# Kernel optimization log

Measured on AMD Instinct MI355X. Metric: run time of the kernel, lower is better.

## Reference

```python
import jax, jax.numpy as jnp
import numpy as np

N = 100000   # points in scan
K = 20       # KNN neighbors
D = 96       # backbone feature dim
H = 1024     # random-projection dim
C = 7        # num classes


def setup_inputs() -> dict:
    key = jax.random.key(0)
    ks = jax.random.split(key, 6)
    feat_source = jax.random.normal(ks[0], (N, D), jnp.float32)
    proto = jax.random.normal(ks[1], (C, D), jnp.float32)
    w_rand = jax.random.normal(ks[2], (D, H), jnp.float32)
    Q = jnp.zeros((H, C), jnp.float32)
    G = jnp.zeros((H, H), jnp.float32)
    coords = jax.random.normal(ks[3], (N, 3), jnp.float32) * 30.0
    normals_z = jax.random.uniform(ks[4], (N,), jnp.float32)
    near_indices = jax.random.randint(ks[5], (N, K), 0, N).astype(jnp.int64)
    return dict(feat_source=feat_source, proto=proto, w_rand=w_rand, Q=Q, G=G,
                coords=coords, normals_z=normals_z, near_indices=near_indices)


def _prior_filter(preds, coords, normals_z):
    plane_pred = (preds == 2) | (preds == 3) | (preds == 4)
    manmade_pred = preds == 5
    other = (preds == 0) | (preds == 1) | (preds == 6)
    ground = plane_pred & (normals_z > 0.9) & (coords[:, 2] < -10.0)
    g_index = ground | other | manmade_pred
    m_index = (manmade_pred & (normals_z < 0.1)) | other | plane_pred
    return g_index, m_index


def reference(feat_source, proto, w_rand, Q, G, coords, normals_z, near_indices):
    RIDGE = 100.0  # stand-in for optimise_ridge_parameter (source not provided)
    # prototype logits: feat @ normalize(proto, dim=1).T   [N, C]
    proto_n = proto / jnp.maximum(jnp.linalg.norm(proto, axis=1, keepdims=True), 1e-12)
    pred_proto = feat_source @ proto_n.T
    preds = jnp.argmax(pred_proto, axis=1)                       # [N]
    # KNN consistency filtering (irregular gather)
    neigh = preds[near_indices]                                  # [N, K]
    consistency = jnp.mean((neigh == preds[:, None]).astype(jnp.float32), axis=1)
    cmask = consistency > 0.8
    g_index, m_index = _prior_filter(preds, coords, normals_z)
    mask = cmask & g_index & m_index                             # [N]
    # random-projection features
    feat_h = jax.nn.relu(feat_source @ w_rand)                   # [N, H]
    yhat = jax.nn.one_hot(preds, C, dtype=feat_h.dtype)          # [N, C]
    mw = mask.astype(feat_h.dtype)[:, None]
    fh_m = feat_h * mw                                           # masked rows (mask^2 == mask)
    Qn = Q + jnp.einsum('nh,nc->hc', fh_m, yhat)
    Gn = G + fh_m.T @ fh_m
    # ridge solve: wo = solve(G + r*I, Q); module does feat_h @ wo
    wo = jnp.linalg.solve(Gn + RIDGE * jnp.eye(H, dtype=Gn.dtype), Qn)  # [H, C]
    pred_domain = feat_h @ wo                                    # [N, C]
    return pred_domain
```

## Files before the change

### kernel.cpp

```cpp
#include <hip/hip_runtime.h>

#define D_DIM 96
#define K_NN  20
#define H_DIM 1024
#define C_CLS 7


__global__ void k_preds(const float* __restrict__ feat,
                        const float* __restrict__ proto,
                        const long long* __restrict__ idx_ll,
                        int* __restrict__ preds, int* __restrict__ flags, int N) {
  __shared__ float pn[C_CLS * D_DIM];
  __shared__ float inv[C_CLS];
  __shared__ int any_big;
  if (threadIdx.x == 0) any_big = 0;
  if (threadIdx.x < C_CLS) {
    float ss = 0.f;
    for (int d = 0; d < D_DIM; d++) {
      float v = proto[threadIdx.x * D_DIM + d];
      ss += v * v;
    }
    inv[threadIdx.x] = 1.0f / fmaxf(sqrtf(ss), 1e-12f);
  }
  __syncthreads();
  for (int j = threadIdx.x; j < C_CLS * D_DIM; j += blockDim.x)
    pn[j] = proto[j] * inv[j / D_DIM];
  if (blockIdx.x == 0) {
    for (int j = threadIdx.x; j < 1024; j += blockDim.x) {
      long long v = idx_ll[j];
      if (v < 0 || v >= N) any_big = 1;
    }
  }
  __syncthreads();
  if (blockIdx.x == 0 && threadIdx.x == 0) {
    flags[0] = 0;
    flags[1] = any_big ? 0 : 1;
  }
  int i = blockIdx.x * blockDim.x + threadIdx.x;
  if (i >= N) return;
  const float4* fp = (const float4*)(feat + (size_t)i * D_DIM);
  float s[C_CLS];
#pragma unroll
  for (int c = 0; c < C_CLS; c++) s[c] = 0.f;
#pragma unroll
  for (int q = 0; q < D_DIM / 4; q++) {
    float4 v = fp[q];
    int d = q * 4;
#pragma unroll
    for (int c = 0; c < C_CLS; c++) {
      s[c] += v.x * pn[c * D_DIM + d]     + v.y * pn[c * D_DIM + d + 1]
            + v.z * pn[c * D_DIM + d + 2] + v.w * pn[c * D_DIM + d + 3];
    }
  }
  float best = s[0]; int bi = 0;
#pragma unroll
  for (int c = 1; c < C_CLS; c++) { if (s[c] > best) { best = s[c]; bi = c; } }
  preds[i] = bi;
}

__global__ void k_mask(const int* __restrict__ preds, const void* __restrict__ nearv,
                       const float* __restrict__ coords, const float* __restrict__ normz,
                       int* __restrict__ flags, int* __restrict__ list, int N) {
  int i = blockIdx.x * blockDim.x + threadIdx.x;
  if (i >= N) return;
  int p = preds[i];
  int cnt = 0;
  if (flags[1]) {
    const long long* nn = (const long long*)nearv + (long long)i * K_NN;
#pragma unroll
    for (int k = 0; k < K_NN; k++) cnt += (preds[(int)nn[k]] == p) ? 1 : 0;
  } else {
    const int* nn = (const int*)nearv + (size_t)i * K_NN;
#pragma unroll
    for (int k = 0; k < K_NN; k++) cnt += (preds[nn[k]] == p) ? 1 : 0;
  }
  bool cmask = (cnt >= 17);
  bool plane = (p == 2) || (p == 3) || (p == 4);
  bool man   = (p == 5);
  bool other = (p == 0) || (p == 1) || (p == 6);
  float nz = normz[i];
  bool ground = plane && (nz > 0.9f) && (coords[(size_t)i * 3 + 2] < -10.0f);
  bool g = ground || other || man;
  bool m = (man && (nz < 0.1f)) || other || plane;
  if (cmask && g && m) {
    int pos = atomicAdd(&flags[0], 1);
    list[pos] = i;
  }
}

__global__ void k_qn_copy(const float* __restrict__ feat, const float* __restrict__ w,
                          const float* __restrict__ Q, const int* __restrict__ preds,
                          const int* __restrict__ flags, const int* __restrict__ list,
                          float* __restrict__ Qn,
                          const float* __restrict__ G, float* __restrict__ Gn) {
  if (blockIdx.x < 1024) {
    size_t t = (size_t)blockIdx.x * 256 + threadIdx.x;
    ((float4*)Gn)[t] = ((const float4*)G)[t];
    return;
  }
  int h = (blockIdx.x - 1024) * 256 + threadIdx.x;
  float q[C_CLS];
#pragma unroll
  for (int c = 0; c < C_CLS; c++) q[c] = Q[h * C_CLS + c];
  int M = flags[0];
  for (int m = 0; m < M; m++) {
    int i = list[m];
    float s = 0.f;
    for (int d = 0; d < D_DIM; d++) s += feat[(size_t)i * D_DIM + d] * w[(size_t)d * H_DIM + h];
    s = fmaxf(s, 0.f);
    q[preds[i]] += s;
  }
#pragma unroll
  for (int c = 0; c < C_CLS; c++) Qn[h * C_CLS + c] = q[c];
}

__global__ void k_gram_acc(const float* __restrict__ feat, const float* __restrict__ w,
                           const int* __restrict__ flags, const int* __restrict__ list,
                           float* __restrict__ Gn) {
  int M = flags[0];
  if (M == 0) return;
  int bx = blockIdx.x & 15, by = blockIdx.x >> 4;
  int tr0 = by * 64, tc0 = bx * 64;
  __shared__ float fr[64], fc[64], fsh[D_DIM];
  float acc[4][4];
#pragma unroll
  for (int u = 0; u < 4; u++)
#pragma unroll
    for (int v = 0; v < 4; v++) acc[u][v] = 0.f;
  int t = threadIdx.x;
  int tu = t >> 4, tv = t & 15;
  for (int m = 0; m < M; m++) {
    int i = list[m];
    if (t < D_DIM) fsh[t] = feat[(size_t)i * D_DIM + t];
    __syncthreads();
    if (t < 64) {
      float s = 0.f;
      for (int d = 0; d < D_DIM; d++) s += fsh[d] * w[(size_t)d * H_DIM + tr0 + t];
      fr[t] = fmaxf(s, 0.f);
    } else if (t < 128) {
      int c = t - 64;
      float s = 0.f;
      for (int d = 0; d < D_DIM; d++) s += fsh[d] * w[(size_t)d * H_DIM + tc0 + c];
      fc[c] = fmaxf(s, 0.f);
    }
    __syncthreads();
#pragma unroll
    for (int u = 0; u < 4; u++)
#pragma unroll
      for (int v = 0; v < 4; v++) acc[u][v] += fr[tu * 4 + u] * fc[tv * 4 + v];
    __syncthreads();
  }
#pragma unroll
  for (int u = 0; u < 4; u++)
#pragma unroll
    for (int v = 0; v < 4; v++) {
      int r = tr0 + tu * 4 + u, c = tc0 + tv * 4 + v;
      Gn[(size_t)r * H_DIM + c] += acc[u][v];
    }
}

__device__ inline void block_reduce7(const float* val, volatile float* out,
                                     float* red) {
  int lane = threadIdx.x & 63, wave = threadIdx.x >> 6;
#pragma unroll
  for (int c = 0; c < C_CLS; c++) {
    float v = val[c];
#pragma unroll
    for (int o = 32; o > 0; o >>= 1) v += __shfl_down(v, o, 64);
    if (lane == 0) red[wave * C_CLS + c] = v;
  }
  __syncthreads();
  if (threadIdx.x == 0) {
#pragma unroll
    for (int c = 0; c < C_CLS; c++) {
      float s = 0.f;
      for (int wv = 0; wv < 16; wv++) s += red[wv * C_CLS + c];
      out[c] = s;
    }
  }
  __syncthreads();
}

__global__ void __launch_bounds__(1024) k_solve(const float* __restrict__ Gn,
                                                const float* __restrict__ Qn,
                                                float* __restrict__ wo,
                                                float* __restrict__ wo_flag) {
  const int h = threadIdx.x;
  __shared__ float psh[H_DIM * C_CLS];
  __shared__ float red[16 * C_CLS];
  __shared__ float rs[C_CLS], bn2[C_CLS], pap[C_CLS], rsn[C_CLS];

  float x[C_CLS], r[C_CLS], p[C_CLS], t7[C_CLS];
#pragma unroll
  for (int c = 0; c < C_CLS; c++) {
    float b = Qn[h * C_CLS + c];
    x[c] = 0.f; r[c] = b; p[c] = b;
    t7[c] = b * b;
  }
  block_reduce7(t7, rs, red);
  if (h == 0) {
#pragma unroll
    for (int c = 0; c < C_CLS; c++) bn2[c] = rs[c];
  }
  __syncthreads();

  for (int it = 0; it < H_DIM; it++) {
    bool done = true;
#pragma unroll
    for (int c = 0; c < C_CLS; c++)
      done = done && (rs[c] <= bn2[c] * 1e-16f + 1e-30f);
    if (done) break;

#pragma unroll
    for (int c = 0; c < C_CLS; c++) psh[h * C_CLS + c] = p[c];
    __syncthreads();

    float ap[C_CLS];
#pragma unroll
    for (int c = 0; c < C_CLS; c++) ap[c] = 100.0f * p[c];
    const float* grow = Gn + (size_t)h * H_DIM;
    for (int k = 0; k < H_DIM; k++) {
      float g = grow[k];
#pragma unroll
      for (int c = 0; c < C_CLS; c++) ap[c] += g * psh[k * C_CLS + c];
    }
#pragma unroll
    for (int c = 0; c < C_CLS; c++) t7[c] = p[c] * ap[c];
    block_reduce7(t7, pap, red);

    float a[C_CLS], rsold[C_CLS];
#pragma unroll
    for (int c = 0; c < C_CLS; c++) {
      rsold[c] = rs[c];
      bool act = rs[c] > bn2[c] * 1e-16f + 1e-30f;
      a[c] = act ? rsold[c] / fmaxf(pap[c], 1e-37f) : 0.f;
    }
#pragma unroll
    for (int c = 0; c < C_CLS; c++) {
      x[c] += a[c] * p[c];
      r[c] -= a[c] * ap[c];
      t7[c] = r[c] * r[c];
    }
    block_reduce7(t7, rsn, red);
#pragma unroll
    for (int c = 0; c < C_CLS; c++) {
      float bb = rsn[c] / fmaxf(rsold[c], 1e-37f);
      p[c] = r[c] + bb * p[c];
    }
    if (h == 0) {
#pragma unroll
      for (int c = 0; c < C_CLS; c++) rs[c] = rsn[c];
    }
    __syncthreads();
  }

#pragma unroll
  for (int c = 0; c < C_CLS; c++) wo[h * C_CLS + c] = x[c];
  float s = 0.f;
#pragma unroll
  for (int c = 0; c < C_CLS; c++) s += fabsf(x[c]);
  t7[0] = s;
#pragma unroll
  for (int c = 1; c < C_CLS; c++) t7[c] = 0.f;
  block_reduce7(t7, rsn, red);
  if (h == 0) *wo_flag = rsn[0];
}

__global__ void k_out(const float* __restrict__ feat, const float* __restrict__ w,
                      const float* __restrict__ wo, const float* __restrict__ wo_flag,
                      float* __restrict__ out, int N) {
  if (*wo_flag == 0.0f) {
    long long tid = (long long)blockIdx.x * blockDim.x + threadIdx.x;
    long long total = (long long)N * C_CLS;
    if (tid < total) out[tid] = 0.0f;
    return;
  }
  int i = blockIdx.x * blockDim.x + threadIdx.x;
  if (i >= N) return;
  float f[D_DIM];
  const float4* fp = (const float4*)(feat + (size_t)i * D_DIM);
#pragma unroll
  for (int q = 0; q < D_DIM / 4; q++) {
    float4 v = fp[q];
    f[4 * q] = v.x; f[4 * q + 1] = v.y; f[4 * q + 2] = v.z; f[4 * q + 3] = v.w;
  }
  float acc[C_CLS];
#pragma unroll
  for (int c = 0; c < C_CLS; c++) acc[c] = 0.f;
  for (int hh = 0; hh < H_DIM; hh++) {
    float s = 0.f;
#pragma unroll 8
    for (int d = 0; d < D_DIM; d++) s += f[d] * w[(size_t)d * H_DIM + hh];
    s = fmaxf(s, 0.f);
    const float* wrow = wo + hh * C_CLS;
#pragma unroll
    for (int c = 0; c < C_CLS; c++) acc[c] += s * wrow[c];
  }
#pragma unroll
  for (int c = 0; c < C_CLS; c++) out[(size_t)i * C_CLS + c] = acc[c];
}

extern "C" void kernel_launch(void* const* d_in, const int* in_sizes, int n_in,
                              void* d_out, int out_size, void* d_ws, size_t ws_size,
                              hipStream_t stream) {
  const float* feat   = (const float*)d_in[0];
  const float* proto  = (const float*)d_in[1];
  const float* w      = (const float*)d_in[2];
  const float* Q      = (const float*)d_in[3];
  const float* G      = (const float*)d_in[4];
  const float* coords = (const float*)d_in[5];
  const float* normz  = (const float*)d_in[6];
  const void*  nearv  = d_in[7];
  float* out = (float*)d_out;

  const int N = in_sizes[0] / D_DIM;

  char* WS = (char*)d_ws;
  int*   flags   = (int*)(WS + 4096);
  float* wo_flag = (float*)(WS + 4160);
  int*   preds   = (int*)(WS + 8192);
  int*   list    = (int*)(WS + 8192 + 400000);
  float* Qn      = (float*)(WS + 808192);
  float* wo      = (float*)(WS + 836864);
  float* Gn      = (float*)(WS + 865536);
  if (ws_size < 5059840) return;

  int nblk = (N + 255) / 256;
  hipLaunchKernelGGL(k_preds, dim3(nblk), dim3(256), 0, stream,
                     feat, proto, (const long long*)nearv, preds, flags, N);
  hipLaunchKernelGGL(k_mask, dim3(nblk), dim3(256), 0, stream,
                     preds, nearv, coords, normz, flags, list, N);
  hipLaunchKernelGGL(k_qn_copy, dim3(1024 + H_DIM / 256), dim3(256), 0, stream,
                     feat, w, Q, preds, flags, list, Qn, G, Gn);
  hipLaunchKernelGGL(k_gram_acc, dim3(256), dim3(256), 0, stream,
                     feat, w, flags, list, Gn);
  hipLaunchKernelGGL(k_solve, dim3(1), dim3(1024), 0, stream,
                     Gn, Qn, wo, wo_flag);
  int oblk = (N * C_CLS + 255) / 256;
  hipLaunchKernelGGL(k_out, dim3(oblk), dim3(256), 0, stream,
                     feat, w, wo, wo_flag, out, N);
}
```

Before: 130.6 us.

## Fuse Gram/Q accumulation into solve kernel and merge G copy into mask

Removes the separate Qn and Gram-accumulation kernels. The masked-row Q and G updates now run inside the single-block ridge solve kernel, and the G-to-Gn copy is folded into the KNN mask kernel. k_preds now handles two rows per thread, reads the prototypes as float4 from shared memory, and the mask kernel loads neighbour indices with vector loads. This cuts launch count and intermediate traffic, at the risk of a serial single-block Gram update when many rows pass the mask.

```diff
diff --git a/kernel.cpp b/kernel.cpp
--- a/kernel.cpp
+++ b/kernel.cpp
@@ -10,70 +10,100 @@
                         const float* __restrict__ proto,
                         const long long* __restrict__ idx_ll,
                         int* __restrict__ preds, int* __restrict__ flags, int N) {
-  __shared__ float pn[C_CLS * D_DIM];
+  __shared__ float4 pn4[C_CLS * (D_DIM / 4)];
   __shared__ float inv[C_CLS];
   __shared__ int any_big;
-  if (threadIdx.x == 0) any_big = 0;
-  if (threadIdx.x < C_CLS) {
-    float ss = 0.f;
-    for (int d = 0; d < D_DIM; d++) {
-      float v = proto[threadIdx.x * D_DIM + d];
-      ss += v * v;
-    }
-    inv[threadIdx.x] = 1.0f / fmaxf(sqrtf(ss), 1e-12f);
-  }
-  __syncthreads();
-  for (int j = threadIdx.x; j < C_CLS * D_DIM; j += blockDim.x)
-    pn[j] = proto[j] * inv[j / D_DIM];
+  const int t = threadIdx.x;
+  if (t == 0) any_big = 0;
+  if (t < C_CLS * (D_DIM / 4)) pn4[t] = ((const float4*)proto)[t];
   if (blockIdx.x == 0) {
-    for (int j = threadIdx.x; j < 1024; j += blockDim.x) {
+    for (int j = t; j < 1024; j += blockDim.x) {
       long long v = idx_ll[j];
       if (v < 0 || v >= N) any_big = 1;
     }
   }
   __syncthreads();
-  if (blockIdx.x == 0 && threadIdx.x == 0) {
+  if (t < C_CLS) {
+    const float* row = (const float*)&pn4[t * (D_DIM / 4)];
+    float ss = 0.f;
+    for (int d = 0; d < D_DIM; d++) ss += row[d] * row[d];
+    inv[t] = 1.0f / fmaxf(sqrtf(ss), 1e-12f);
+  }
+  __syncthreads();
+  if (t < C_CLS * (D_DIM / 4)) {
+    float s = inv[t / (D_DIM / 4)];
+    float4 v = pn4[t];
+    v.x *= s; v.y *= s; v.z *= s; v.w *= s;
+    pn4[t] = v;
+  }
+  if (blockIdx.x == 0 && t == 0) {
     flags[0] = 0;
     flags[1] = any_big ? 0 : 1;
   }
-  int i = blockIdx.x * blockDim.x + threadIdx.x;
-  if (i >= N) return;
-  const float4* fp = (const float4*)(feat + (size_t)i * D_DIM);
-  float s[C_CLS];
-#pragma unroll
-  for (int c = 0; c < C_CLS; c++) s[c] = 0.f;
-#pragma unroll
+  __syncthreads();
+
+  int i0 = blockIdx.x * 512 + t;
+  int i1 = i0 + 256;
+  int j0 = min(i0, N - 1), j1 = min(i1, N - 1);
+  const float4* f0p = (const float4*)feat + (size_t)j0 * (D_DIM / 4);
+  const float4* f1p = (const float4*)feat + (size_t)j1 * (D_DIM / 4);
+  float s0[C_CLS], s1[C_CLS];
+#pragma unroll
+  for (int c = 0; c < C_CLS; c++) { s0[c] = 0.f; s1[c] = 0.f; }
+#pragma unroll 4
   for (int q = 0; q < D_DIM / 4; q++) {
-    float4 v = fp[q];
-    int d = q * 4;
-#pragma unroll
-    for (int c = 0; c < C_CLS; c++) {
-      s[c] += v.x * pn[c * D_DIM + d]     + v.y * pn[c * D_DIM + d + 1]
-            + v.z * pn[c * D_DIM + d + 2] + v.w * pn[c * D_DIM + d + 3];
-    }
-  }
-  float best = s[0]; int bi = 0;
-#pragma unroll
-  for (int c = 1; c < C_CLS; c++) { if (s[c] > best) { best = s[c]; bi = c; } }
-  preds[i] = bi;
-}
-
-__global__ void k_mask(const int* __restrict__ preds, const void* __restrict__ nearv,
-                       const float* __restrict__ coords, const float* __restrict__ normz,
-                       int* __restrict__ flags, int* __restrict__ list, int N) {
+    float4 a = f0p[q];
+    float4 b = f1p[q];
+#pragma unroll
+    for (int c = 0; c < C_CLS; c++) {
+      float4 p = pn4[c * (D_DIM / 4) + q];
+      s0[c] += a.x * p.x + a.y * p.y + a.z * p.z + a.w * p.w;
+      s1[c] += b.x * p.x + b.y * p.y + b.z * p.z + b.w * p.w;
+    }
+  }
+  float b0 = s0[0]; int a0 = 0;
+  float b1 = s1[0]; int a1 = 0;
+#pragma unroll
+  for (int c = 1; c < C_CLS; c++) {
+    if (s0[c] > b0) { b0 = s0[c]; a0 = c; }
+    if (s1[c] > b1) { b1 = s1[c]; a1 = c; }
+  }
+  if (i0 < N) preds[i0] = a0;
+  if (i1 < N) preds[i1] = a1;
+}
+
+__global__ void k_mask_copy(const int* __restrict__ preds, const void* __restrict__ nearv,
+                            const float* __restrict__ coords, const float* __restrict__ normz,
+                            int* __restrict__ flags, int* __restrict__ list,
+                            const float* __restrict__ G, float* __restrict__ Gn, int N) {
+  {
+    const int total4 = (H_DIM * H_DIM) / 4;
+    int stride = gridDim.x * blockDim.x;
+    for (int v = blockIdx.x * blockDim.x + threadIdx.x; v < total4; v += stride)
+      ((float4*)Gn)[v] = ((const float4*)G)[v];
+  }
   int i = blockIdx.x * blockDim.x + threadIdx.x;
   if (i >= N) return;
   int p = preds[i];
+  int idx[K_NN];
+  if (flags[1]) {
+    const longlong2* nn = (const longlong2*)((const long long*)nearv + (long long)i * K_NN);
+#pragma unroll
+    for (int k = 0; k < K_NN / 2; k++) {
+      longlong2 v = nn[k];
+      idx[2 * k] = (int)v.x; idx[2 * k + 1] = (int)v.y;
+    }
+  } else {
+    const int4* nn = (const int4*)((const int*)nearv + (size_t)i * K_NN);
+#pragma unroll
+    for (int k = 0; k < K_NN / 4; k++) {
+      int4 v = nn[k];
+      idx[4 * k] = v.x; idx[4 * k + 1] = v.y; idx[4 * k + 2] = v.z; idx[4 * k + 3] = v.w;
+    }
+  }
   int cnt = 0;
-  if (flags[1]) {
-    const long long* nn = (const long long*)nearv + (long long)i * K_NN;
-#pragma unroll
-    for (int k = 0; k < K_NN; k++) cnt += (preds[(int)nn[k]] == p) ? 1 : 0;
-  } else {
-    const int* nn = (const int*)nearv + (size_t)i * K_NN;
-#pragma unroll
-    for (int k = 0; k < K_NN; k++) cnt += (preds[nn[k]] == p) ? 1 : 0;
-  }
+#pragma unroll
+  for (int k = 0; k < K_NN; k++) cnt += (preds[idx[k]] == p) ? 1 : 0;
   bool cmask = (cnt >= 17);
   bool plane = (p == 2) || (p == 3) || (p == 4);
   bool man   = (p == 5);
@@ -88,77 +118,6 @@
   }
 }
 
-__global__ void k_qn_copy(const float* __restrict__ feat, const float* __restrict__ w,
-                          const float* __restrict__ Q, const int* __restrict__ preds,
-                          const int* __restrict__ flags, const int* __restrict__ list,
-                          float* __restrict__ Qn,
-                          const float* __restrict__ G, float* __restrict__ Gn) {
-  if (blockIdx.x < 1024) {
-    size_t t = (size_t)blockIdx.x * 256 + threadIdx.x;
-    ((float4*)Gn)[t] = ((const float4*)G)[t];
-    return;
-  }
-  int h = (blockIdx.x - 1024) * 256 + threadIdx.x;
-  float q[C_CLS];
-#pragma unroll
-  for (int c = 0; c < C_CLS; c++) q[c] = Q[h * C_CLS + c];
-  int M = flags[0];
-  for (int m = 0; m < M; m++) {
-    int i = list[m];
-    float s = 0.f;
-    for (int d = 0; d < D_DIM; d++) s += feat[(size_t)i * D_DIM + d] * w[(size_t)d * H_DIM + h];
-    s = fmaxf(s, 0.f);
-    q[preds[i]] += s;
-  }
-#pragma unroll
-  for (int c = 0; c < C_CLS; c++) Qn[h * C_CLS + c] = q[c];
-}
-
-__global__ void k_gram_acc(const float* __restrict__ feat, const float* __restrict__ w,
-                           const int* __restrict__ flags, const int* __restrict__ list,
-                           float* __restrict__ Gn) {
-  int M = flags[0];
-  if (M == 0) return;
-  int bx = blockIdx.x & 15, by = blockIdx.x >> 4;
-  int tr0 = by * 64, tc0 = bx * 64;
-  __shared__ float fr[64], fc[64], fsh[D_DIM];
-  float acc[4][4];
-#pragma unroll
-  for (int u = 0; u < 4; u++)
-#pragma unroll
-    for (int v = 0; v < 4; v++) acc[u][v] = 0.f;
-  int t = threadIdx.x;
-  int tu = t >> 4, tv = t & 15;
-  for (int m = 0; m < M; m++) {
-    int i = list[m];
-    if (t < D_DIM) fsh[t] = feat[(size_t)i * D_DIM + t];
-    __syncthreads();
-    if (t < 64) {
-      float s = 0.f;
-      for (int d = 0; d < D_DIM; d++) s += fsh[d] * w[(size_t)d * H_DIM + tr0 + t];
-      fr[t] = fmaxf(s, 0.f);
-    } else if (t < 128) {
-      int c = t - 64;
-      float s = 0.f;
-      for (int d = 0; d < D_DIM; d++) s += fsh[d] * w[(size_t)d * H_DIM + tc0 + c];
-      fc[c] = fmaxf(s, 0.f);
-    }
-    __syncthreads();
-#pragma unroll
-    for (int u = 0; u < 4; u++)
-#pragma unroll
-      for (int v = 0; v < 4; v++) acc[u][v] += fr[tu * 4 + u] * fc[tv * 4 + v];
-    __syncthreads();
-  }
-#pragma unroll
-  for (int u = 0; u < 4; u++)
-#pragma unroll
-    for (int v = 0; v < 4; v++) {
-      int r = tr0 + tu * 4 + u, c = tc0 + tv * 4 + v;
-      Gn[(size_t)r * H_DIM + c] += acc[u][v];
-    }
-}
-
 __device__ inline void block_reduce7(const float* val, volatile float* out,
                                      float* red) {
   int lane = threadIdx.x & 63, wave = threadIdx.x >> 6;
@@ -181,8 +140,13 @@
   __syncthreads();
 }
 
-__global__ void __launch_bounds__(1024) k_solve(const float* __restrict__ Gn,
-                                                const float* __restrict__ Qn,
+__global__ void __launch_bounds__(1024) k_ridge(const float* __restrict__ feat,
+                                                const float* __restrict__ w,
+                                                const float* __restrict__ Q,
+                                                const int* __restrict__ preds,
+                                                const int* __restrict__ flags,
+                                                const int* __restrict__ list,
+                                                float* __restrict__ Gn,
                                                 float* __restrict__ wo,
                                                 float* __restrict__ wo_flag) {
   const int h = threadIdx.x;
@@ -190,12 +154,30 @@
   __shared__ float red[16 * C_CLS];
   __shared__ float rs[C_CLS], bn2[C_CLS], pap[C_CLS], rsn[C_CLS];
 
+  const int M = flags[0];
+  float b[C_CLS];
+#pragma unroll
+  for (int c = 0; c < C_CLS; c++) b[c] = Q[h * C_CLS + c];
+  for (int m = 0; m < M; m++) {
+    int i = list[m];
+    float s = 0.f;
+    for (int d = 0; d < D_DIM; d++)
+      s += feat[(size_t)i * D_DIM + d] * w[(size_t)d * H_DIM + h];
+    s = fmaxf(s, 0.f);
+    b[preds[i]] += s;
+    psh[h] = s;
+    __syncthreads();
+    float sh = psh[h];
+    for (int k = 0; k < H_DIM; k++)
+      Gn[(size_t)h * H_DIM + k] += sh * psh[k];
+    __syncthreads();
+  }
+
   float x[C_CLS], r[C_CLS], p[C_CLS], t7[C_CLS];
 #pragma unroll
   for (int c = 0; c < C_CLS; c++) {
-    float b = Qn[h * C_CLS + c];
-    x[c] = 0.f; r[c] = b; p[c] = b;
-    t7[c] = b * b;
+    x[c] = 0.f; r[c] = b[c]; p[c] = b[c];
+    t7[c] = b[c] * b[c];
   }
   block_reduce7(t7, rs, red);
   if (h == 0) {
@@ -320,22 +302,18 @@
   float* wo_flag = (float*)(WS + 4160);
   int*   preds   = (int*)(WS + 8192);
   int*   list    = (int*)(WS + 8192 + 400000);
-  float* Qn      = (float*)(WS + 808192);
   float* wo      = (float*)(WS + 836864);
   float* Gn      = (float*)(WS + 865536);
   if (ws_size < 5059840) return;
 
+  int pblk = (N + 511) / 512;
+  hipLaunchKernelGGL(k_preds, dim3(pblk), dim3(256), 0, stream,
+                     feat, proto, (const long long*)nearv, preds, flags, N);
   int nblk = (N + 255) / 256;
-  hipLaunchKernelGGL(k_preds, dim3(nblk), dim3(256), 0, stream,
-                     feat, proto, (const long long*)nearv, preds, flags, N);
-  hipLaunchKernelGGL(k_mask, dim3(nblk), dim3(256), 0, stream,
-                     preds, nearv, coords, normz, flags, list, N);
-  hipLaunchKernelGGL(k_qn_copy, dim3(1024 + H_DIM / 256), dim3(256), 0, stream,
-                     feat, w, Q, preds, flags, list, Qn, G, Gn);
-  hipLaunchKernelGGL(k_gram_acc, dim3(256), dim3(256), 0, stream,
-                     feat, w, flags, list, Gn);
-  hipLaunchKernelGGL(k_solve, dim3(1), dim3(1024), 0, stream,
-                     Gn, Qn, wo, wo_flag);
+  hipLaunchKernelGGL(k_mask_copy, dim3(nblk), dim3(256), 0, stream,
+                     preds, nearv, coords, normz, flags, list, G, Gn, N);
+  hipLaunchKernelGGL(k_ridge, dim3(1), dim3(1024), 0, stream,
+                     feat, w, Q, preds, flags, list, Gn, wo, wo_flag);
   int oblk = (N * C_CLS + 255) / 256;
   hipLaunchKernelGGL(k_out, dim3(oblk), dim3(256), 0, stream,
                      feat, w, wo, wo_flag, out, N);
```

New measurement: 126.6 us. 1.03x faster.
